# Kernel tuning notes

Measured on AMD Instinct MI355X. Metric: run time of the kernel, lower is better.

Reference implementation:

```python
import jax, jax.numpy as jnp
import numpy as np

VIGILANCE = 0.75


def setup_inputs() -> dict:
    key = jax.random.key(0)
    k1, k2 = jax.random.split(key)
    N, D, C = 1024, 256, 512
    x = jax.random.uniform(k1, (N, D), dtype=jnp.float32)
    categories = jax.random.uniform(k2, (C, D), dtype=jnp.float32)
    return {"x": x, "categories": categories}


def reference(x, categories):
    # Fuzzy ART choice/match: match[n, c] = sum_d min(x[n,d], w[c,d]) / sum_d x[n,d]
    # x: [N, D], categories: [C, D] -> min-broadcast [N, C, D], reduce over D.
    fuzzy_and = jnp.minimum(x[:, None, :], categories[None, :, :]).sum(-1)  # [N, C]
    match = fuzzy_and / x.sum(-1, keepdims=True)                            # [N, C]
    # Vigilance gating: scores below vigilance stay 0 (as in compute_match_scores)
    match_scores = jnp.where(match >= VIGILANCE, match, jnp.zeros_like(match))
    indices = jnp.argmax(match_scores, axis=1)  # torch.max(dim=1) indices
    return (match_scores, indices)
```

## Files before the change

### kernel.cpp

```cpp
#include <hip/hip_runtime.h>

#define BM 64
#define BN 64
#define BK 32
#define VIG 0.75f

__global__ __launch_bounds__(256) void fuzzy_scores_kernel(
    const float* __restrict__ x, const float* __restrict__ w,
    float* __restrict__ out0, float* __restrict__ wsbuf,
    int N, int C, int D, int kchunk)
{
    __shared__ float sA[BK * BM];
    __shared__ float sB[BK * BN];

    const int t  = threadIdx.x;
    const int cx = t & 15;
    const int ry = t >> 4;
    const int bx = blockIdx.x, by = blockIdx.y, bz = blockIdx.z;
    const int d0 = bz * kchunk;

    float acc[4][4];
#pragma unroll
    for (int i = 0; i < 4; ++i)
#pragma unroll
        for (int j = 0; j < 4; ++j) acc[i][j] = 0.f;

    for (int kb = 0; kb < kchunk; kb += BK) {
        __syncthreads();
#pragma unroll
        for (int l = 0; l < 2; ++l) {
            const int q  = l * 256 + t;
            const int rr = q >> 3;
            const int kq = (q & 7) << 2;
            const int c3 = q & 3;
            const int gb = ((((rr >> 2) ^ c3) << 2) | (rr & 3));

            const float4 v = *(const float4*)(x + (size_t)(bx * BM + rr) * D + d0 + kb + kq);
            sA[(kq + 0) * BM + gb] = v.x;
            sA[(kq + 1) * BM + gb] = v.y;
            sA[(kq + 2) * BM + gb] = v.z;
            sA[(kq + 3) * BM + gb] = v.w;

            const float4 u = *(const float4*)(w + (size_t)(by * BN + rr) * D + d0 + kb + kq);
            sB[(kq + 0) * BN + gb] = u.x;
            sB[(kq + 1) * BN + gb] = u.y;
            sB[(kq + 2) * BN + gb] = u.z;
            sB[(kq + 3) * BN + gb] = u.w;
        }
        __syncthreads();

#pragma unroll
        for (int k = 0; k < BK; ++k) {
            const int c3 = (k >> 2) & 3;
            const float4 a = *(const float4*)&sA[k * BM + ((ry ^ c3) << 2)];
            const float4 b = *(const float4*)&sB[k * BN + ((cx ^ c3) << 2)];
            const float av[4] = {a.x, a.y, a.z, a.w};
            const float bv[4] = {b.x, b.y, b.z, b.w};
#pragma unroll
            for (int i = 0; i < 4; ++i)
#pragma unroll
                for (int j = 0; j < 4; ++j)
                    acc[i][j] += fminf(av[i], bv[j]);
        }
    }

    float* dst = (bz == 0) ? out0 : (wsbuf + (size_t)(bz - 1) * N * C);
    const int col = by * BN + (cx << 2);
#pragma unroll
    for (int i = 0; i < 4; ++i) {
        const int row = bx * BM + (ry << 2) + i;
        *(float4*)(dst + (size_t)row * C + col) =
            make_float4(acc[i][0], acc[i][1], acc[i][2], acc[i][3]);
    }
}

__global__ __launch_bounds__(256) void fuzzy_finish_kernel(
    const float* __restrict__ x, float* __restrict__ out,
    const float* __restrict__ wsbuf, int N, int C, int D, int ksplit)
{
    const int n = blockIdx.x;
    const int t = threadIdx.x;
    const int lane = t & 63;
    const int wid  = t >> 6;

    float v = x[(size_t)n * D + t];
#pragma unroll
    for (int s = 1; s < 64; s <<= 1) v += __shfl_xor(v, s);
    __shared__ float wsum[4];
    if (lane == 0) wsum[wid] = v;
    __syncthreads();
    const float sumx = wsum[0] + wsum[1] + wsum[2] + wsum[3];

    float best = -1.f;
    int   bidx = 0;
    for (int j = 0; j < C; j += 256) {
        const int c = j + t;
        const size_t off = (size_t)n * C + c;
        float raw = out[off];
        for (int p = 1; p < ksplit; ++p)
            raw += wsbuf[(size_t)(p - 1) * N * C + off];
        const float m = raw / sumx;
        const float s = (m >= VIG) ? m : 0.f;
        out[off] = s;
        if (s > best) { best = s; bidx = c; }
    }

#pragma unroll
    for (int s2 = 1; s2 < 64; s2 <<= 1) {
        const float ov = __shfl_xor(best, s2);
        const int   oi = __shfl_xor(bidx, s2);
        if (ov > best || (ov == best && oi < bidx)) { best = ov; bidx = oi; }
    }
    __shared__ float bvs[4];
    __shared__ int   bis[4];
    if (lane == 0) { bvs[wid] = best; bis[wid] = bidx; }
    __syncthreads();
    if (t == 0) {
        for (int w2 = 1; w2 < 4; ++w2) {
            if (bvs[w2] > best || (bvs[w2] == best && bis[w2] < bidx)) {
                best = bvs[w2];
                bidx = bis[w2];
            }
        }
        out[(size_t)N * C + n] = (float)bidx;
    }
}

extern "C" void kernel_launch(void* const* d_in, const int* in_sizes, int n_in,
                              void* d_out, int out_size, void* d_ws, size_t ws_size,
                              hipStream_t stream) {
    const float* x = (const float*)d_in[0];
    const float* w = (const float*)d_in[1];
    float* out = (float*)d_out;
    float* ws  = (float*)d_ws;

    const int D = 256;
    const int N = in_sizes[0] / D;
    const int C = in_sizes[1] / D;

    const size_t partial_bytes = (size_t)N * C * sizeof(float);
    int ksplit = 1;
    if (ws_size >= 3 * partial_bytes)      ksplit = 4;
    else if (ws_size >= partial_bytes)     ksplit = 2;
    const int kchunk = D / ksplit;

    dim3 grid(N / BM, C / BN, ksplit);
    fuzzy_scores_kernel<<<grid, 256, 0, stream>>>(x, w, out, ws, N, C, D, kchunk);
    fuzzy_finish_kernel<<<N, 256, 0, stream>>>(x, out, ws, N, C, D, ksplit);
}
```

Before: 74.02 us.

## Fuse min-sum, normalization and argmax into a single per-row-block kernel

Replaces the tiled two-kernel split-K design with a single fused kernel. Each block handles 4 rows of x, and each of 512 threads handles one category. Every thread streams its category's weight row from global memory and reads the x values with uniform (broadcast) loads. The kernel computes the row sums, the vigilance gating and the argmax in-block, which removes the workspace partials and the second launch. The cost is that shared-memory tiling and data reuse are dropped: each block rereads the full weight matrix, and thread loads of w are strided by the row length, so they are not coalesced.

```diff
diff --git a/kernel.cpp b/kernel.cpp
--- a/kernel.cpp
+++ b/kernel.cpp
@@ -1,128 +1,85 @@
 #include <hip/hip_runtime.h>
 
-#define BM 64
-#define BN 64
-#define BK 32
-#define VIG 0.75f
+#define VIG   0.75f
+#define DD    256
+#define ROWS  4
 
-__global__ __launch_bounds__(256) void fuzzy_scores_kernel(
+__global__ __launch_bounds__(512, 2) void fuzzy_fused_kernel(
     const float* __restrict__ x, const float* __restrict__ w,
-    float* __restrict__ out0, float* __restrict__ wsbuf,
-    int N, int C, int D, int kchunk)
+    float* __restrict__ out, int N, int C)
 {
-    __shared__ float sA[BK * BM];
-    __shared__ float sB[BK * BN];
+    const int t  = threadIdx.x;
+    const int r0 = blockIdx.x * ROWS;
 
-    const int t  = threadIdx.x;
-    const int cx = t & 15;
-    const int ry = t >> 4;
-    const int bx = blockIdx.x, by = blockIdx.y, bz = blockIdx.z;
-    const int d0 = bz * kchunk;
+    __shared__ float part[8];
+    __shared__ float redv[ROWS][8];
+    __shared__ int   redi[ROWS][8];
 
-    float acc[4][4];
+    {
+        const int rid = t >> 7;
+        const int j   = t & 127;
+        const float* xr = x + (size_t)(r0 + rid) * DD;
+        float v = xr[j] + xr[j + 128];
 #pragma unroll
-    for (int i = 0; i < 4; ++i)
+        for (int s = 1; s < 64; s <<= 1) v += __shfl_xor(v, s);
+        if ((t & 63) == 0) part[t >> 6] = v;
+    }
+    __syncthreads();
+    float sumx[ROWS];
 #pragma unroll
-        for (int j = 0; j < 4; ++j) acc[i][j] = 0.f;
+    for (int r = 0; r < ROWS; ++r) sumx[r] = part[2 * r] + part[2 * r + 1];
 
-    for (int kb = 0; kb < kchunk; kb += BK) {
-        __syncthreads();
+    float acc[ROWS] = {0.f, 0.f, 0.f, 0.f};
+    const float* wp = w + (size_t)t * DD;
+    const float* xb = x + (size_t)r0 * DD;
+
+    for (int k = 0; k < DD; k += 16) {
+        const float4 w0 = *(const float4*)(wp + k);
+        const float4 w1 = *(const float4*)(wp + k + 4);
+        const float4 w2 = *(const float4*)(wp + k + 8);
+        const float4 w3 = *(const float4*)(wp + k + 12);
+        float wv[16];
+        wv[0]  = w0.x; wv[1]  = w0.y; wv[2]  = w0.z; wv[3]  = w0.w;
+        wv[4]  = w1.x; wv[5]  = w1.y; wv[6]  = w1.z; wv[7]  = w1.w;
+        wv[8]  = w2.x; wv[9]  = w2.y; wv[10] = w2.z; wv[11] = w2.w;
+        wv[12] = w3.x; wv[13] = w3.y; wv[14] = w3.z; wv[15] = w3.w;
 #pragma unroll
-        for (int l = 0; l < 2; ++l) {
-            const int q  = l * 256 + t;
-            const int rr = q >> 3;
-            const int kq = (q & 7) << 2;
-            const int c3 = q & 3;
-            const int gb = ((((rr >> 2) ^ c3) << 2) | (rr & 3));
-
-            const float4 v = *(const float4*)(x + (size_t)(bx * BM + rr) * D + d0 + kb + kq);
-            sA[(kq + 0) * BM + gb] = v.x;
-            sA[(kq + 1) * BM + gb] = v.y;
-            sA[(kq + 2) * BM + gb] = v.z;
-            sA[(kq + 3) * BM + gb] = v.w;
-
-            const float4 u = *(const float4*)(w + (size_t)(by * BN + rr) * D + d0 + kb + kq);
-            sB[(kq + 0) * BN + gb] = u.x;
-            sB[(kq + 1) * BN + gb] = u.y;
-            sB[(kq + 2) * BN + gb] = u.z;
-            sB[(kq + 3) * BN + gb] = u.w;
-        }
-        __syncthreads();
-
+        for (int r = 0; r < ROWS; ++r) {
+            const float* xr = xb + r * DD + k;
 #pragma unroll
-        for (int k = 0; k < BK; ++k) {
-            const int c3 = (k >> 2) & 3;
-            const float4 a = *(const float4*)&sA[k * BM + ((ry ^ c3) << 2)];
-            const float4 b = *(const float4*)&sB[k * BN + ((cx ^ c3) << 2)];
-            const float av[4] = {a.x, a.y, a.z, a.w};
-            const float bv[4] = {b.x, b.y, b.z, b.w};
-#pragma unroll
-            for (int i = 0; i < 4; ++i)
-#pragma unroll
-                for (int j = 0; j < 4; ++j)
-                    acc[i][j] += fminf(av[i], bv[j]);
+            for (int kk = 0; kk < 16; ++kk)
+                acc[r] += fminf(xr[kk], wv[kk]);
         }
     }
 
-    float* dst = (bz == 0) ? out0 : (wsbuf + (size_t)(bz - 1) * N * C);
-    const int col = by * BN + (cx << 2);
 #pragma unroll
-    for (int i = 0; i < 4; ++i) {
-        const int row = bx * BM + (ry << 2) + i;
-        *(float4*)(dst + (size_t)row * C + col) =
-            make_float4(acc[i][0], acc[i][1], acc[i][2], acc[i][3]);
+    for (int r = 0; r < ROWS; ++r) {
+        const float m = acc[r] / sumx[r];
+        const float s = (m >= VIG) ? m : 0.f;
+        out[(size_t)(r0 + r) * C + t] = s;
+
+        float bv = s;
+        int   bi = t;
+#pragma unroll
+        for (int sh = 1; sh < 64; sh <<= 1) {
+            const float ov = __shfl_xor(bv, sh);
+            const int   oi = __shfl_xor(bi, sh);
+            if (ov > bv || (ov == bv && oi < bi)) { bv = ov; bi = oi; }
+        }
+        if ((t & 63) == 0) { redv[r][t >> 6] = bv; redi[r][t >> 6] = bi; }
     }
-}
-
-__global__ __launch_bounds__(256) void fuzzy_finish_kernel(
-    const float* __restrict__ x, float* __restrict__ out,
-    const float* __restrict__ wsbuf, int N, int C, int D, int ksplit)
-{
-    const int n = blockIdx.x;
-    const int t = threadIdx.x;
-    const int lane = t & 63;
-    const int wid  = t >> 6;
-
-    float v = x[(size_t)n * D + t];
+    __syncthreads();
+    if (t < ROWS) {
+        float bv = redv[t][0];
+        int   bi = redi[t][0];
 #pragma unroll
-    for (int s = 1; s < 64; s <<= 1) v += __shfl_xor(v, s);
-    __shared__ float wsum[4];
-    if (lane == 0) wsum[wid] = v;
-    __syncthreads();
-    const float sumx = wsum[0] + wsum[1] + wsum[2] + wsum[3];
-
-    float best = -1.f;
-    int   bidx = 0;
-    for (int j = 0; j < C; j += 256) {
-        const int c = j + t;
-        const size_t off = (size_t)n * C + c;
-        float raw = out[off];
-        for (int p = 1; p < ksplit; ++p)
-            raw += wsbuf[(size_t)(p - 1) * N * C + off];
-        const float m = raw / sumx;
-        const float s = (m >= VIG) ? m : 0.f;
-        out[off] = s;
-        if (s > best) { best = s; bidx = c; }
-    }
-
-#pragma unroll
-    for (int s2 = 1; s2 < 64; s2 <<= 1) {
-        const float ov = __shfl_xor(best, s2);
-        const int   oi = __shfl_xor(bidx, s2);
-        if (ov > best || (ov == best && oi < bidx)) { best = ov; bidx = oi; }
-    }
-    __shared__ float bvs[4];
-    __shared__ int   bis[4];
-    if (lane == 0) { bvs[wid] = best; bis[wid] = bidx; }
-    __syncthreads();
-    if (t == 0) {
-        for (int w2 = 1; w2 < 4; ++w2) {
-            if (bvs[w2] > best || (bvs[w2] == best && bis[w2] < bidx)) {
-                best = bvs[w2];
-                bidx = bis[w2];
+        for (int q = 1; q < 8; ++q) {
+            if (redv[t][q] > bv || (redv[t][q] == bv && redi[t][q] < bi)) {
+                bv = redv[t][q];
+                bi = redi[t][q];
             }
         }
-        out[(size_t)N * C + n] = (float)bidx;
+        out[(size_t)N * C + r0 + t] = (float)bi;
     }
 }
 
@@ -132,19 +89,10 @@
     const float* x = (const float*)d_in[0];
     const float* w = (const float*)d_in[1];
     float* out = (float*)d_out;
-    float* ws  = (float*)d_ws;
+    (void)d_ws; (void)ws_size;
 
-    const int D = 256;
-    const int N = in_sizes[0] / D;
-    const int C = in_sizes[1] / D;
+    const int N = in_sizes[0] / DD;
+    const int C = in_sizes[1] / DD;
 
-    const size_t partial_bytes = (size_t)N * C * sizeof(float);
-    int ksplit = 1;
-    if (ws_size >= 3 * partial_bytes)      ksplit = 4;
-    else if (ws_size >= partial_bytes)     ksplit = 2;
-    const int kchunk = D / ksplit;
-
-    dim3 grid(N / BM, C / BN, ksplit);
-    fuzzy_scores_kernel<<<grid, 256, 0, stream>>>(x, w, out, ws, N, C, D, kchunk);
-    fuzzy_finish_kernel<<<N, 256, 0, stream>>>(x, out, ws, N, C, D, ksplit);
+    fuzzy_fused_kernel<<<N / ROWS, C, 0, stream>>>(x, w, out, N, C);
 }
```

Result: no change. 74.25 us (+0.3%).
